# Performance work log

Measured on AMD Instinct MI355X. Metric: run time of the kernel, lower is better.

## Reference

```python
import jax, jax.numpy as jnp
from jax import lax
import numpy as np

B, C_IN, H, W = 8, 1024, 64, 64
DI, C_OUT = 512, 1024
BN_EPS = 1e-5


def setup_inputs() -> dict:
    key = jax.random.key(0)
    ks = jax.random.split(key, 5)
    std = 0.01  # torch init.normal_(std=0.01)
    return {
        "x": jax.random.normal(ks[0], (B, C_IN, H, W), jnp.float32),
        "theta_w": jax.random.normal(ks[1], (DI, C_IN), jnp.float32) * std,
        "theta_b": jnp.zeros((DI,), jnp.float32),
        "phi_w": jax.random.normal(ks[2], (DI, C_IN), jnp.float32) * std,
        "phi_b": jnp.zeros((DI,), jnp.float32),
        "g_w": jax.random.normal(ks[3], (DI, C_IN), jnp.float32) * std,
        "g_b": jnp.zeros((DI,), jnp.float32),
        "out_w": jax.random.normal(ks[4], (C_OUT, DI), jnp.float32) * std,
        "out_b": jnp.zeros((C_OUT,), jnp.float32),
        "bn_w": jnp.ones((C_OUT,), jnp.float32),
        "bn_b": jnp.zeros((C_OUT,), jnp.float32),
    }


def _conv1x1(x, w, b):
    # x: [b,c,h,w], w: [o,c] -> [b,o,h,w]
    return jnp.einsum('bchw,oc->bohw', x, w) + b[None, :, None, None]


def reference(x, theta_w, theta_b, phi_w, phi_b, g_w, g_b, out_w, out_b, bn_w, bn_b):
    b, c, h, w = x.shape
    di = theta_w.shape[0]

    theta = _conv1x1(x, theta_w, theta_b).reshape(b, di, h * w)  # [b,di,N]

    # MaxPool2d(kernel=2, stride=2)
    pool = lax.reduce_window(x, -jnp.inf, lax.max,
                             (1, 1, 2, 2), (1, 1, 2, 2), 'VALID')
    phi = _conv1x1(pool, phi_w, phi_b).reshape(b, di, -1)   # [b,di,M]
    g = _conv1x1(pool, g_w, g_b).reshape(b, di, -1)          # [b,di,M]

    # scaled dot-product attention: scores [b,N,M]
    scores = jnp.einsum('bdn,bdm->bnm', theta, phi) * (di ** -0.5)
    p = jax.nn.softmax(scores, axis=-1)

    # t_x = g @ p^T  -> [b,di,N]
    t = jnp.einsum('bdm,bnm->bdn', g, p).reshape(b, di, h, w)

    y = _conv1x1(t, out_w, out_b)  # [b,C_out,h,w]

    # BatchNorm2d (training mode: batch statistics, biased variance)
    mean = jnp.mean(y, axis=(0, 2, 3), keepdims=True)
    var = jnp.var(y, axis=(0, 2, 3), keepdims=True)
    y = (y - mean) * lax.rsqrt(var + BN_EPS)
    y = y * bn_w[None, :, None, None] + bn_b[None, :, None, None]

    return y + x
```

## Files before the change

kernel.cpp:

```cpp
#include <hip/hip_runtime.h>
#include <cstdint>

typedef unsigned short u16;
typedef __attribute__((ext_vector_type(4))) unsigned short u16x4;
typedef __attribute__((ext_vector_type(8))) short short8;
typedef __attribute__((ext_vector_type(4))) float f32x4;

#define DI 512
#define CIN 1024
#define NPIX 4096
#define MPIX 1024

__device__ __forceinline__ float bf2f(u16 u) {
  union { unsigned int i; float f; } v; v.i = ((unsigned int)u) << 16; return v.f;
}
__device__ __forceinline__ u16 f2bf(float f) {
  union { float f; unsigned int i; } v; v.f = f;
  unsigned int r = v.i + 0x7fffu + ((v.i >> 16) & 1u);
  return (u16)(r >> 16);
}
__device__ __forceinline__ void unpack8(uint4 v, float* f) {
  union { unsigned int i; float f; } u;
  u.i = v.x << 16;          f[0] = u.f;
  u.i = v.x & 0xffff0000u;  f[1] = u.f;
  u.i = v.y << 16;          f[2] = u.f;
  u.i = v.y & 0xffff0000u;  f[3] = u.f;
  u.i = v.z << 16;          f[4] = u.f;
  u.i = v.z & 0xffff0000u;  f[5] = u.f;
  u.i = v.w << 16;          f[6] = u.f;
  u.i = v.w & 0xffff0000u;  f[7] = u.f;
}

__device__ __forceinline__ void gload16(const u16* g, u16* l) {
  __builtin_amdgcn_global_load_lds(
      (const __attribute__((address_space(1))) void*)g,
      (__attribute__((address_space(3))) void*)l, 16, 0, 0);
}

template<int N> __device__ __forceinline__ void wait_vmcnt() {
  asm volatile("s_waitcnt vmcnt(%0)" :: "n"(N) : "memory");
}
__device__ __forceinline__ void phase_begin() {
  __builtin_amdgcn_s_barrier();
  __builtin_amdgcn_sched_barrier(0);
  asm volatile("" ::: "memory");
}
__device__ __forceinline__ void phase_end() {
  asm volatile("s_waitcnt lgkmcnt(0)" ::: "memory");
  __builtin_amdgcn_sched_barrier(0);
  __builtin_amdgcn_s_barrier();
  __builtin_amdgcn_sched_barrier(0);
}

__global__ __launch_bounds__(256) void cvt4_kernel(
    const float* __restrict__ s0, const float* __restrict__ s1,
    const float* __restrict__ s2, const float* __restrict__ s3,
    u16* __restrict__ d0, u16* __restrict__ d1,
    u16* __restrict__ d2, u16* __restrict__ d3) {
  int i = blockIdx.x * 256 + threadIdx.x;
  int sel = i >> 17;
  int j = i & 131071;
  const float* src = sel == 0 ? s0 : sel == 1 ? s1 : sel == 2 ? s2 : s3;
  u16* dst = sel == 0 ? d0 : sel == 1 ? d1 : sel == 2 ? d2 : d3;
  float4 v = *(const float4*)(src + (long)j * 4);
  u16x4 w;
  w[0] = f2bf(v.x); w[1] = f2bf(v.y); w[2] = f2bf(v.z); w[3] = f2bf(v.w);
  *(u16x4*)(dst + (long)j * 4) = w;
}

__global__ __launch_bounds__(256) void transpose_pool_kernel(
    const float* __restrict__ x, u16* __restrict__ xT, u16* __restrict__ poolT) {
  __shared__ u16 tile[64][136];
  const int b = blockIdx.z;
  const int n0 = blockIdx.x * 128, c0 = blockIdx.y * 64;
  const float* xb = x + (long)b * CIN * NPIX;
  u16* xTb = xT + (long)b * NPIX * CIN;
  const int t = threadIdx.x;
  const int tc = t >> 5, tn = (t & 31) * 4;
  #pragma unroll
  for (int i = 0; i < 8; i++) {
    int c = tc + i * 8;
    float4 v = *(const float4*)(xb + (long)(c0 + c) * NPIX + n0 + tn);
    u16x4 w;
    w[0] = f2bf(v.x); w[1] = f2bf(v.y); w[2] = f2bf(v.z); w[3] = f2bf(v.w);
    *(u16x4*)&tile[c][tn] = w;
  }
  __syncthreads();
  const int tn2 = t >> 4, tc2 = (t & 15) * 4;
  #pragma unroll
  for (int i = 0; i < 8; i++) {
    int n = tn2 + i * 16;
    u16x4 w;
    w[0] = tile[tc2 + 0][n];
    w[1] = tile[tc2 + 1][n];
    w[2] = tile[tc2 + 2][n];
    w[3] = tile[tc2 + 3][n];
    *(u16x4*)(xTb + (long)(n0 + n) * CIN + c0 + tc2) = w;
  }
  const int j = t & 31, g = t >> 5;
  u16 r[8] __attribute__((aligned(16)));
  #pragma unroll
  for (int k = 0; k < 8; k++) {
    const int c = g * 8 + k;
    const unsigned d0 = *(const unsigned*)&tile[c][2 * j];
    const unsigned d1 = *(const unsigned*)&tile[c][64 + 2 * j];
    float m0 = fmaxf(bf2f((u16)(d0 & 0xffffu)), bf2f((u16)(d0 >> 16)));
    float m1 = fmaxf(bf2f((u16)(d1 & 0xffffu)), bf2f((u16)(d1 >> 16)));
    r[k] = f2bf(fmaxf(m0, m1));
  }
  *(uint4*)(poolT + ((long)b * MPIX + blockIdx.x * 32 + j) * CIN + c0 + g * 8) =
      *(uint4*)r;
}

template<int OM, bool HAS_BIAS, bool HAS_SHIFT, bool HAS_EXP, bool HAS_PSUM2,
         bool HAS_CSP>
__global__ __launch_bounds__(512, 2)
void gemm256(const u16* __restrict__ A, const u16* __restrict__ B,
             void* __restrict__ Cv,
             const float* __restrict__ bias, long sBias,
             const float* __restrict__ cs, long sCS,
             const float* __restrict__ shift, long sShift,
             float* __restrict__ psum_out,
             float scale, int M, int N, int K, long sA, long sB, long sC)
{
  A += blockIdx.z * sA;
  B += blockIdx.z * sB;
  if (HAS_BIAS) bias += blockIdx.z * sBias;
  if (HAS_CSP) cs += blockIdx.z * sCS;
  if (HAS_SHIFT) shift += blockIdx.z * sShift;
  const int bm = blockIdx.y * 256, bn = blockIdx.x * 256;
  __shared__ __align__(16) u16 smem[65536];
  __shared__ float psum[4][256];
  __shared__ float psumq[4][256];
  __shared__ float invs[256];
  const int tid = threadIdx.x;
  const int lane = tid & 63, wave = tid >> 6;
  const int wr = wave >> 2, wc = wave & 3;
  const int lr = lane & 15, q = lane >> 4;
  f32x4 acc[8][4] = {};

  if (HAS_CSP) {
    if (tid < 256) {
      float ssum = 0.f;
      #pragma unroll
      for (int xx = 0; xx < 4; xx++) ssum += cs[xx * 4096 + bn + tid];
      invs[tid] = 1.0f / ssum;
    }
    wait_vmcnt<0>();
    __builtin_amdgcn_sched_barrier(0);
  }

  const int srow = 32 * wave + (lane >> 2);
  const int sk = (((lane & 3) ^ ((lane >> 3) & 3))) * 8;
  const u16* Abase = A + ((long)bm + srow) * K + sk;
  const u16* Bbase = B + ((long)bn + srow) * K + sk;
  const int rswz = (q ^ ((lr >> 1) & 3)) * 8;
  const int aoff = (wr * 128 + lr) * 32 + rswz;
  const int boff = 16384 + (wc * 64 + lr) * 32 + rswz;

#define SA(T_, KK_) { const u16* g_ = Abase + (long)(T_) * 64 + (KK_) * 32; \
    u16* d_ = &smem[(((T_) & 1)) * 32768 + (KK_) * 8192 + wave * 1024]; \
    gload16(g_, d_); gload16(g_ + 16 * (long)K, d_ + 512); }
#define SB(T_, KK_) { const u16* g_ = Bbase + (long)(T_) * 64 + (KK_) * 32; \
    u16* d_ = &smem[(((T_) & 1)) * 32768 + 16384 + (KK_) * 8192 + wave * 1024]; \
    gload16(g_, d_); gload16(g_ + 16 * (long)K, d_ + 512); }
#define CQ(SLOT, KK, RI0, LOADBV) { \
    const int qb_ = (SLOT) * 32768 + (KK) * 8192; \
    if (LOADBV) { \
      _Pragma("unroll") \
      for (int ci_ = 0; ci_ < 4; ci_++) \
        bv[ci_] = *(const short8*)&smem[qb_ + boff + ci_ * 512]; \
    } \
    short8 av_[4]; \
    _Pragma("unroll") \
    for (int r_ = 0; r_ < 4; r_++) \
      av_[r_] = *(const short8*)&smem[qb_ + aoff + ((RI0) + r_) * 512]; \
    __builtin_amdgcn_s_setprio(1); \
    _Pragma("unroll") \
    for (int r_ = 0; r_ < 4; r_++) \
      _Pragma("unroll") \
      for (int ci_ = 0; ci_ < 4; ci_++) \
        acc[(RI0) + r_][ci_] = __builtin_amdgcn_mfma_f32_16x16x32_bf16( \
            av_[r_], bv[ci_], acc[(RI0) + r_][ci_], 0, 0, 0); \
    __builtin_amdgcn_s_setprio(0); }
#define PH(VM, STG, SLOT, KK, RI0, LOADBV) \
    STG; wait_vmcnt<VM>(); phase_begin(); CQ(SLOT, KK, RI0, LOADBV); phase_end();

  const int niter2 = K >> 7;
  short8 bv[4];

  SA(0, 0); SB(0, 0); SA(0, 1); SB(0, 1); SA(1, 0); SB(1, 0);

  for (int u = 0; u < niter2 - 1; ++u) {
    const int t1 = 2 * u + 1, t2 = 2 * u + 2, t3 = 2 * u + 3;
    PH(10, SA(t1, 1), 0, 0, 0, 1)
    PH(10, SB(t1, 1), 0, 0, 4, 0)
    PH(10, SA(t2, 0), 0, 1, 0, 1)
    PH(10, SB(t2, 0), 0, 1, 4, 0)
    PH(10, SA(t2, 1), 1, 0, 0, 1)
    PH(10, SB(t2, 1), 1, 0, 4, 0)
    PH(10, SA(t3, 0), 1, 1, 0, 1)
    PH(10, SB(t3, 0), 1, 1, 4, 0)
  }
  {
    const int t1 = 2 * (niter2 - 1) + 1;
    PH(10, SA(t1, 1), 0, 0, 0, 1)
    PH(10, SB(t1, 1), 0, 0, 4, 0)
    PH(8,  ((void)0), 0, 1, 0, 1)
    PH(6,  ((void)0), 0, 1, 4, 0)
    PH(4,  ((void)0), 1, 0, 0, 1)
    PH(2,  ((void)0), 1, 0, 4, 0)
    PH(0,  ((void)0), 1, 1, 0, 1)
    PH(0,  ((void)0), 1, 1, 4, 0)
  }
#undef SA
#undef SB
#undef CQ
#undef PH

  __syncthreads();

  const int dr = (lane >> 4) * 4;
  float invc[4];
  if (HAS_CSP) {
    #pragma unroll
    for (int ci = 0; ci < 4; ci++) invc[ci] = invs[wc * 64 + ci * 16 + lr];
  }
  float rowsum[8][4], rowsq[8][4];
  if (HAS_EXP || HAS_PSUM2) {
    #pragma unroll
    for (int ri = 0; ri < 8; ri++)
      #pragma unroll
      for (int r = 0; r < 4; r++) { rowsum[ri][r] = 0.f; rowsq[ri][r] = 0.f; }
  }
  #pragma unroll
  for (int ri = 0; ri < 8; ri++) {
    const int rowl = wr * 128 + ri * 16 + dr;
    const int rowb = bm + rowl;
    float bvs[4] = {0.f, 0.f, 0.f, 0.f};
    float shv[4] = {0.f, 0.f, 0.f, 0.f};
    if (HAS_BIAS) {
      #pragma unroll
      for (int r = 0; r < 4; r++) bvs[r] = bias[rowb + r];
    }
    if (HAS_SHIFT) {
      #pragma unroll
      for (int r = 0; r < 4; r++) shv[r] = shift[rowb + r];
    }
    #pragma unroll
    for (int ci = 0; ci < 4; ci++) {
      const int coll = wc * 64 + ci * 16 + lr;
      float v[4];
      #pragma unroll
      for (int r = 0; r < 4; r++) {
        float tv = acc[ri][ci][r] * scale;
        if (HAS_CSP) tv *= invc[ci];
        if (HAS_SHIFT) tv -= shv[r];
        if (HAS_BIAS) tv += bvs[r];
        if (HAS_EXP) tv = expf(tv);
        if (HAS_EXP || HAS_PSUM2) rowsum[ri][r] += tv;
        if (HAS_PSUM2) rowsq[ri][r] += tv * tv;
        v[r] = tv;
      }
      if (OM == 1) {
        u16x4 w;
        #pragma unroll
        for (int r = 0; r < 4; r++) w[r] = f2bf(v[r]);
        unsigned bo = (unsigned)((coll * 256 + rowl) * 2) ^ ((coll & 7) << 4);
        *(u16x4*)((char*)smem + bo) = w;
      } else {
        #pragma unroll
        for (int r = 0; r < 4; r++) smem[(rowl + r) * 256 + coll] = f2bf(v[r]);
      }
    }
  }
  if (HAS_EXP || HAS_PSUM2) {
    #pragma unroll
    for (int msk = 1; msk < 16; msk <<= 1)
      #pragma unroll
      for (int ri = 0; ri < 8; ri++)
        #pragma unroll
        for (int r = 0; r < 4; r++) {
          rowsum[ri][r] += __shfl_xor(rowsum[ri][r], msk);
          if (HAS_PSUM2) rowsq[ri][r] += __shfl_xor(rowsq[ri][r], msk);
        }
    if ((lane & 15) == 0) {
      #pragma unroll
      for (int ri = 0; ri < 8; ri++)
        #pragma unroll
        for (int r = 0; r < 4; r++) {
          psum[wc][wr * 128 + ri * 16 + dr + r] = rowsum[ri][r];
          if (HAS_PSUM2) psumq[wc][wr * 128 + ri * 16 + dr + r] = rowsq[ri][r];
        }
    }
  }
  __syncthreads();
  u16* C = (u16*)Cv + blockIdx.z * sC;
  if (OM == 1) {
    #pragma unroll
    for (int i = 0; i < 16; i++) {
      const int chunk = i * 512 + tid;
      const int coll = chunk >> 5, rq = chunk & 31;
      unsigned bo = (unsigned)(coll * 512 + rq * 16) ^ ((coll & 7) << 4);
      uint4 w = *(const uint4*)((const char*)smem + bo);
      *(uint4*)(C + (long)(bn + coll) * M + bm + rq * 8) = w;
    }
  } else {
    #pragma unroll
    for (int i = 0; i < 16; i++) {
      const int chunk = i * 512 + tid;
      const int row = chunk >> 5, cq = chunk & 31;
      uint4 w = *(const uint4*)(smem + row * 256 + cq * 8);
      *(uint4*)(C + (long)(bm + row) * N + bn + cq * 8) = w;
    }
  }
  if ((HAS_EXP || HAS_PSUM2) && tid < 256) {
    if (HAS_EXP)
      psum_out[((long)blockIdx.z * gridDim.x + blockIdx.x) * 4096 + bm + tid] =
          psum[0][tid] + psum[1][tid] + psum[2][tid] + psum[3][tid];
    if (HAS_PSUM2) {
      const long blk = ((long)blockIdx.z * gridDim.y + blockIdx.y) * gridDim.x
                       + blockIdx.x;
      psum_out[blk * 512 + tid] =
          psum[0][tid] + psum[1][tid] + psum[2][tid] + psum[3][tid];
      psum_out[blk * 512 + 256 + tid] =
          psumq[0][tid] + psumq[1][tid] + psumq[2][tid] + psumq[3][tid];
    }
  }
}

template<int OM, bool HAS_BIAS, bool HAS_CS, bool HAS_SHIFT, bool HAS_EXP,
         bool HAS_PSUM2, bool HAS_CSP>
__global__ __launch_bounds__(256)
void gemm_tn(const u16* __restrict__ A, const u16* __restrict__ B,
             void* __restrict__ Cv, void* __restrict__ Cv2,
             const float* __restrict__ bias, const float* __restrict__ bias2,
             long sBias,
             const float* __restrict__ cs, long sCS,
             const float* __restrict__ shift, long sShift,
             float* __restrict__ psum_out,
             float scale, int M, int N, int K, long sA, long sB, long sC)
{
  A += blockIdx.z * sA;
  B += blockIdx.z * sB;
  if (HAS_BIAS) bias += blockIdx.z * sBias;
  if (HAS_CS || HAS_CSP) cs += blockIdx.z * sCS;
  if (HAS_SHIFT) shift += blockIdx.z * sShift;
  const int bm = blockIdx.y * 128;
  const int bn = blockIdx.x * 128;
  __shared__ __align__(16) u16 smem[128 * 128];
  u16* As = smem;
  u16* Bs = smem + 128 * 64;
  __shared__ float psum[4][128];
  const int tid = threadIdx.x;
  const int lane = tid & 63;
  const int wave = tid >> 6;
  const int wm = (wave >> 1) * 64;
  const int wn = (wave & 1) * 64;
  const int lr = lane & 15;
  const int q  = lane >> 4;
  const int sxor = lane & 7;
  const bool gps = (OM == 3) && (bm >= 512);
  f32x4 acc[4][4] = {};

  if (HAS_CSP) {
    if (tid < 128) {
      float s = 0.f;
      #pragma unroll
      for (int xx = 0; xx < 8; xx++) s += cs[xx * 4096 + bn + tid];
      psum[0][tid] = 1.0f / s;
    }
  }

  const int swz = ((lane & 7) ^ (lane >> 3)) * 8;
  const long grow = 32 * wave + (lane >> 3);
  const u16* Ag = A + ((long)bm + grow) * K + swz;
  const u16* Bg = B + ((long)bn + grow) * K + swz;

  for (int kt = 0; kt < K; kt += 64) {
    __syncthreads();
    #pragma unroll
    for (int i = 0; i < 4; i++) {
      gload16(Ag + (long)(8 * i) * K + kt, &As[(wave * 4 + i) * 512]);
      gload16(Bg + (long)(8 * i) * K + kt, &Bs[(wave * 4 + i) * 512]);
    }
    __syncthreads();
    #pragma unroll
    for (int kk = 0; kk < 2; kk++) {
      short8 av[4], bv[4];
      #pragma unroll
      for (int mi = 0; mi < 4; mi++)
        av[mi] = *(const short8*)&As[(wm + mi * 16 + lr) * 64 +
                                     (((kk << 2) + q) ^ sxor) * 8];
      #pragma unroll
      for (int ni = 0; ni < 4; ni++)
        bv[ni] = *(const short8*)&Bs[(wn + ni * 16 + lr) * 64 +
                                     (((kk << 2) + q) ^ sxor) * 8];
      #pragma unroll
      for (int mi = 0; mi < 4; mi++) {
        #pragma unroll
        for (int ni = 0; ni < 4; ni++)
          acc[mi][ni] = __builtin_amdgcn_mfma_f32_16x16x32_bf16(
              av[mi], bv[ni], acc[mi][ni], 0, 0, 0);
      }
    }
  }

  float invc[4];
  if (HAS_CSP) {
    #pragma unroll
    for (int ni = 0; ni < 4; ni++) invc[ni] = psum[0][wn + ni * 16 + lr];
  }
  __syncthreads();
  const int dr = (lane >> 4) * 4;
  const bool trans_out = (OM == 1) || (OM == 3 && !gps);
  float rowsum[4][4];
  float rowsq[4][4];
  if (HAS_EXP || HAS_PSUM2 || gps) {
    #pragma unroll
    for (int mi = 0; mi < 4; mi++)
      #pragma unroll
      for (int r = 0; r < 4; r++) { rowsum[mi][r] = 0.f; rowsq[mi][r] = 0.f; }
  }
  const float* bp = (OM == 3 && gps) ? bias2 - 512 : bias;
  #pragma unroll
  for (int mi = 0; mi < 4; mi++) {
    const int rowl = wm + mi * 16 + dr;
    const int rowb = bm + rowl;
    float bvs[4] = {0.f, 0.f, 0.f, 0.f};
    float shv[4] = {0.f, 0.f, 0.f, 0.f};
    if (HAS_BIAS) {
      #pragma unroll
      for (int r = 0; r < 4; r++) bvs[r] = bp[rowb + r];
    }
    if (HAS_SHIFT) {
      #pragma unroll
      for (int r = 0; r < 4; r++) shv[r] = shift[rowb + r];
    }
    #pragma unroll
    for (int ni = 0; ni < 4; ni++) {
      const int coll = wn + ni * 16 + lr;
      const float csv = HAS_CSP ? invc[ni] : (HAS_CS ? cs[bn + coll] : 1.0f);
      float v[4];
      #pragma unroll
      for (int r = 0; r < 4; r++) {
        float t = acc[mi][ni][r] * scale;
        if (HAS_CS || HAS_CSP) t *= csv;
        if (HAS_SHIFT) t -= shv[r];
        if (HAS_BIAS) t += bvs[r];
        if (HAS_EXP) t = expf(t);
        if (HAS_EXP || HAS_PSUM2 || gps) rowsum[mi][r] += t;
        if (HAS_PSUM2) rowsq[mi][r] += t * t;
        v[r] = t;
      }
      if (trans_out) {
        u16x4 w;
        #pragma unroll
        for (int r = 0; r < 4; r++) w[r] = f2bf(v[r]);
        unsigned bo = (unsigned)((coll * 128 + rowl) * 2) ^ ((coll & 7) << 4);
        *(u16x4*)((char*)smem + bo) = w;
      } else {
        #pragma unroll
        for (int r = 0; r < 4; r++) smem[(rowl + r) * 128 + coll] = f2bf(v[r]);
      }
    }
  }
  if (HAS_EXP || HAS_PSUM2 || gps) {
    #pragma unroll
    for (int msk = 1; msk < 16; msk <<= 1)
      #pragma unroll
      for (int mi = 0; mi < 4; mi++)
        #pragma unroll
        for (int r = 0; r < 4; r++) {
          rowsum[mi][r] += __shfl_xor(rowsum[mi][r], msk);
          if (HAS_PSUM2) rowsq[mi][r] += __shfl_xor(rowsq[mi][r], msk);
        }
    if ((lane & 15) == 0) {
      #pragma unroll
      for (int mi = 0; mi < 4; mi++)
        #pragma unroll
        for (int r = 0; r < 4; r++) {
          psum[wave & 1][wm + mi * 16 + dr + r] = rowsum[mi][r];
          if (HAS_PSUM2) psum[2 + (wave & 1)][wm + mi * 16 + dr + r] = rowsq[mi][r];
        }
    }
  }
  __syncthreads();
  if (trans_out) {
    const int Ms = (OM == 3) ? 512 : M;
    u16* C = (u16*)Cv + blockIdx.z * sC;
    #pragma unroll
    for (int i = 0; i < 8; i++) {
      const int chunk = i * 256 + tid;
      const int coll = chunk >> 4, rq = chunk & 15;
      unsigned bo = (unsigned)(coll * 256 + rq * 16) ^ ((coll & 7) << 4);
      uint4 w = *(const uint4*)((const char*)smem + bo);
      *(uint4*)(C + (long)(bn + coll) * Ms + bm + rq * 8) = w;
    }
  } else {
    u16* C = (OM == 3) ? (u16*)Cv2 + blockIdx.z * sC : (u16*)Cv + blockIdx.z * sC;
    const int rbase = (OM == 3) ? bm - 512 : bm;
    #pragma unroll
    for (int i = 0; i < 8; i++) {
      const int chunk = i * 256 + tid;
      const int row = chunk >> 4, cq = chunk & 15;
      uint4 w = *(const uint4*)(smem + row * 128 + cq * 8);
      *(uint4*)(C + (long)(rbase + row) * N + bn + cq * 8) = w;
    }
  }
  if (HAS_EXP || HAS_PSUM2 || gps) {
    if (tid < 128) {
      if (HAS_EXP)
        psum_out[((long)blockIdx.z * gridDim.x + blockIdx.x) * 4096 + bm + tid] =
            psum[0][tid] + psum[1][tid];
      if (HAS_PSUM2) {
        const long blk = ((long)blockIdx.z * gridDim.y + blockIdx.y) * gridDim.x
                         + blockIdx.x;
        psum_out[blk * 256 + tid] = psum[0][tid] + psum[1][tid];
        psum_out[blk * 256 + 128 + tid] = psum[2][tid] + psum[3][tid];
      }
      if (gps)
        psum_out[((long)blockIdx.z * gridDim.x + blockIdx.x) * 512 +
                 (bm - 512) + tid] = psum[0][tid] + psum[1][tid];
    }
  }
}

__global__ __launch_bounds__(256) void gbar_kernel(const float* __restrict__ g_ps,
                                                   float* __restrict__ gbar) {
  const int idx = blockIdx.x * 256 + threadIdx.x;
  const int b = idx >> 9, d = idx & 511;
  const float* p = g_ps + (long)b * 8 * 512 + d;
  float s = 0.f;
  #pragma unroll
  for (int xx = 0; xx < 8; xx++) s += p[(long)xx * 512];
  gbar[idx] = s * (1.0f / 1024.0f);
}

__global__ __launch_bounds__(256) void c0_kernel(const float* __restrict__ out_w,
                                                 const float* __restrict__ out_b,
                                                 const float* __restrict__ gbar,
                                                 float* __restrict__ c0) {
  const int idx = blockIdx.x * 4 + (threadIdx.x >> 6);
  const int lane = threadIdx.x & 63;
  const int b = idx >> 10, c = idx & 1023;
  const int d0 = lane * 8;
  float4 w0 = *(const float4*)(out_w + (long)c * DI + d0);
  float4 w1 = *(const float4*)(out_w + (long)c * DI + d0 + 4);
  float4 g0 = *(const float4*)(gbar + (long)b * DI + d0);
  float4 g1 = *(const float4*)(gbar + (long)b * DI + d0 + 4);
  float s = w0.x * g0.x + w0.y * g0.y + w0.z * g0.z + w0.w * g0.w
          + w1.x * g1.x + w1.y * g1.y + w1.z * g1.z + w1.w * g1.w;
  #pragma unroll
  for (int off = 32; off > 0; off >>= 1) s += __shfl_xor(s, off);
  if (lane == 0) c0[idx] = out_b[c] + s;
}

__global__ __launch_bounds__(256) void stats2_kernel(const float* __restrict__ partial,
                                                     const float* __restrict__ c0,
                                                     float* __restrict__ stats) {
  const int co = blockIdx.x * 256 + threadIdx.x;
  const int by = co >> 8, r = co & 255;
  float sd = 0.f, sd2 = 0.f, sbc = 0.f;
  for (int b = 0; b < 8; b++) {
    float sb = 0.f, qb = 0.f;
    #pragma unroll
    for (int bx = 0; bx < 16; bx++) {
      const long blk = (((long)b * 4 + by) * 16 + bx) * 512;
      sb += partial[blk + r];
      qb += partial[blk + 256 + r];
    }
    sd += sb; sd2 += qb;
    sbc += c0[b * 1024 + co] * sb;
  }
  float sc0 = 0.f, sc02 = 0.f;
  #pragma unroll
  for (int b = 0; b < 8; b++) {
    float c = c0[b * 1024 + co];
    sc0 += c; sc02 += c * c;
  }
  stats[co] = 4096.0f * sc0 + sd;
  stats[1024 + co] = 4096.0f * sc02 + 2.0f * sbc + sd2;
}

__global__ __launch_bounds__(256) void final_kernel(const u16* __restrict__ dy,
    const float* __restrict__ x, const float* __restrict__ stats,
    const float* __restrict__ c0,
    const float* __restrict__ bnw, const float* __restrict__ bnb,
    float* __restrict__ out) {
  const int bc = blockIdx.x;
  const int co = bc & 1023;
  const float mean = stats[co] * (1.0f / 32768.0f);
  const float var = stats[1024 + co] * (1.0f / 32768.0f) - mean * mean;
  const float inv = rsqrtf(var + 1e-5f) * bnw[co];
  const float addc = bnb[co] - mean * inv + c0[bc] * inv;
  const long base = (long)bc * 4096;
  const int t = threadIdx.x;
  #pragma unroll
  for (int i = 0; i < 2; i++) {
    const long off = base + (long)(i * 256 + t) * 8;
    uint4 v = *(const uint4*)(dy + off);
    float f[8]; unpack8(v, f);
    const float4 x0 = *(const float4*)(x + off);
    const float4 x1 = *(const float4*)(x + off + 4);
    float4 o0, o1;
    o0.x = f[0] * inv + addc + x0.x;
    o0.y = f[1] * inv + addc + x0.y;
    o0.z = f[2] * inv + addc + x0.z;
    o0.w = f[3] * inv + addc + x0.w;
    o1.x = f[4] * inv + addc + x1.x;
    o1.y = f[5] * inv + addc + x1.y;
    o1.z = f[6] * inv + addc + x1.z;
    o1.w = f[7] * inv + addc + x1.w;
    *(float4*)(out + off) = o0;
    *(float4*)(out + off + 4) = o1;
  }
}

extern "C" void kernel_launch(void* const* d_in, const int* in_sizes, int n_in,
                              void* d_out, int out_size, void* d_ws, size_t ws_size,
                              hipStream_t stream) {
  (void)in_sizes; (void)n_in; (void)out_size; (void)ws_size;
  const float* x       = (const float*)d_in[0];
  const float* theta_w = (const float*)d_in[1];
  const float* theta_b = (const float*)d_in[2];
  const float* phi_w   = (const float*)d_in[3];
  const float* phi_b   = (const float*)d_in[4];
  const float* g_w     = (const float*)d_in[5];
  const float* g_b     = (const float*)d_in[6];
  const float* out_w   = (const float*)d_in[7];
  const float* out_b   = (const float*)d_in[8];
  const float* bn_w    = (const float*)d_in[9];
  const float* bn_b    = (const float*)d_in[10];
  float* out = (float*)d_out;
  char* ws = (char*)d_ws;
  const size_t MB = 1024 * 1024;

  u16* xT     = (u16*)(ws + 0 * MB);
  u16* poolT  = (u16*)(ws + 64 * MB);
  u16* w_th   = (u16*)(ws + 80 * MB);
  u16* w_ph   = (u16*)(ws + 81 * MB);
  u16* w_g    = (u16*)(ws + 82 * MB);
  u16* thetaT = (u16*)(ws + 84 * MB);
  u16* phiT   = (u16*)(ws + 116 * MB);
  u16* g_n    = (u16*)(ws + 124 * MB);
  u16* e      = (u16*)(ws + 132 * MB);
  u16* tT     = (u16*)(ws + 196 * MB);
  u16* w_out  = (u16*)(ws + 228 * MB);
  float* gbar  = (float*)(ws + 229 * MB);
  float* c0b   = (float*)(ws + 229 * MB + 16384);
  float* stats = (float*)(ws + 229 * MB + 49152);
  float* partial = (float*)(ws + 230 * MB);
  float* partial2 = (float*)(ws + 231 * MB);
  float* g_ps = (float*)(ws + 233 * MB);
  u16* dy = xT;

  cvt4_kernel<<<2048, 256, 0, stream>>>(theta_w, phi_w, g_w, out_w,
                                        w_th, w_ph, w_g, w_out);
  transpose_pool_kernel<<<dim3(32, 16, 8), 256, 0, stream>>>(x, xT, poolT);
  gemm256<1, true, false, false, false, false>
      <<<dim3(16, 2, 8), 512, 0, stream>>>(
      w_th, xT, thetaT, theta_b, 0L, nullptr, 0L, nullptr, 0L, nullptr,
      1.0f, 512, 4096, 1024, 0L, (long)NPIX * CIN, (long)NPIX * DI);
  gemm_tn<3, true, false, false, false, false, false>
      <<<dim3(8, 8, 8), 256, 0, stream>>>(
      w_ph, poolT, phiT, g_n, phi_b, g_b, 0L, nullptr, 0L, nullptr, 0L,
      g_ps, 1.0f, 1024, 1024, 1024, 0L, (long)MPIX * CIN, (long)MPIX * DI);
  gbar_kernel<<<16, 256, 0, stream>>>(g_ps, gbar);
  c0_kernel<<<2048, 256, 0, stream>>>(out_w, out_b, gbar, c0b);
  gemm256<0, false, false, true, false, false>
      <<<dim3(4, 16, 8), 512, 0, stream>>>(
      thetaT, phiT, e, nullptr, 0L, nullptr, 0L, nullptr, 0L, partial,
      0.044194173824159216f, 4096, 1024, 512,
      (long)NPIX * DI, (long)MPIX * DI, (long)NPIX * MPIX);
  gemm256<1, false, true, false, false, true>
      <<<dim3(16, 2, 8), 512, 0, stream>>>(
      g_n, e, tT, nullptr, 0L, partial, 16384L, gbar, 512L, nullptr,
      1.0f, 512, 4096, 1024,
      (long)DI * MPIX, (long)NPIX * MPIX, (long)NPIX * DI);
  gemm256<0, false, false, false, true, false>
      <<<dim3(16, 4, 8), 512, 0, stream>>>(
      w_out, tT, dy, nullptr, 0L, nullptr, 0L, nullptr, 0L, partial2,
      1.0f, 1024, 4096, 512, 0L, (long)NPIX * DI, (long)1024 * NPIX);
  stats2_kernel<<<4, 256, 0, stream>>>(partial2, c0b, stats);
  final_kernel<<<8192, 256, 0, stream>>>(dy, x, stats, c0b, bn_w, bn_b, out);
}
```

Baseline: 344.7 us.

## Fuse BN stats reduction into final kernel, swizzle epilogue LDS, use fast exp

Removes the separate stats2 launch. Each final_kernel block now reduces its channel's partial sums and sums of squares with wave shuffles, then broadcasts the scale and shift through shared memory. The row-major epilogue staging in both GEMM kernels gets an XOR swizzle on the column index to reduce LDS bank conflicts, and expf is replaced with __expf in the softmax-exp epilogue. The trade is redundant stats work: each of the 8192 blocks repeats its channel's reduction, so every channel is reduced 8 times, and it adds two block barriers before the elementwise pass.

Result: faster. 337.8 us (-2.0%).

```diff
diff --git a/kernel.cpp b/kernel.cpp
--- a/kernel.cpp
+++ b/kernel.cpp
@@ -257,7 +257,7 @@
         if (HAS_CSP) tv *= invc[ci];
         if (HAS_SHIFT) tv -= shv[r];
         if (HAS_BIAS) tv += bvs[r];
-        if (HAS_EXP) tv = expf(tv);
+        if (HAS_EXP) tv = __expf(tv);
         if (HAS_EXP || HAS_PSUM2) rowsum[ri][r] += tv;
         if (HAS_PSUM2) rowsq[ri][r] += tv * tv;
         v[r] = tv;
@@ -270,7 +270,10 @@
         *(u16x4*)((char*)smem + bo) = w;
       } else {
         #pragma unroll
-        for (int r = 0; r < 4; r++) smem[(rowl + r) * 256 + coll] = f2bf(v[r]);
+        for (int r = 0; r < 4; r++) {
+          const int row = rowl + r;
+          smem[row * 256 + (coll ^ (((row >> 2) & 3) << 4))] = f2bf(v[r]);
+        }
       }
     }
   }
@@ -310,7 +313,8 @@
     for (int i = 0; i < 16; i++) {
       const int chunk = i * 512 + tid;
       const int row = chunk >> 5, cq = chunk & 31;
-      uint4 w = *(const uint4*)(smem + row * 256 + cq * 8);
+      const int cbase = (cq * 8) ^ (((row >> 2) & 3) << 4);
+      uint4 w = *(const uint4*)(smem + row * 256 + cbase);
       *(uint4*)(C + (long)(bm + row) * N + bn + cq * 8) = w;
     }
   }
@@ -448,7 +452,7 @@
         if (HAS_CS || HAS_CSP) t *= csv;
         if (HAS_SHIFT) t -= shv[r];
         if (HAS_BIAS) t += bvs[r];
-        if (HAS_EXP) t = expf(t);
+        if (HAS_EXP) t = __expf(t);
         if (HAS_EXP || HAS_PSUM2 || gps) rowsum[mi][r] += t;
         if (HAS_PSUM2) rowsq[mi][r] += t * t;
         v[r] = t;
@@ -461,7 +465,10 @@
         *(u16x4*)((char*)smem + bo) = w;
       } else {
         #pragma unroll
-        for (int r = 0; r < 4; r++) smem[(rowl + r) * 128 + coll] = f2bf(v[r]);
+        for (int r = 0; r < 4; r++) {
+          const int row = rowl + r;
+          smem[row * 128 + (coll ^ (((row >> 2) & 3) << 4))] = f2bf(v[r]);
+        }
       }
     }
   }
@@ -504,7 +511,8 @@
     for (int i = 0; i < 8; i++) {
       const int chunk = i * 256 + tid;
       const int row = chunk >> 4, cq = chunk & 15;
-      uint4 w = *(const uint4*)(smem + row * 128 + cq * 8);
+      const int cbase = (cq * 8) ^ (((row >> 2) & 3) << 4);
+      uint4 w = *(const uint4*)(smem + row * 128 + cbase);
       *(uint4*)(C + (long)(rbase + row) * N + bn + cq * 8) = w;
     }
   }
@@ -556,46 +564,57 @@
   if (lane == 0) c0[idx] = out_b[c] + s;
 }
 
-__global__ __launch_bounds__(256) void stats2_kernel(const float* __restrict__ partial,
-                                                     const float* __restrict__ c0,
-                                                     float* __restrict__ stats) {
-  const int co = blockIdx.x * 256 + threadIdx.x;
-  const int by = co >> 8, r = co & 255;
-  float sd = 0.f, sd2 = 0.f, sbc = 0.f;
-  for (int b = 0; b < 8; b++) {
-    float sb = 0.f, qb = 0.f;
-    #pragma unroll
-    for (int bx = 0; bx < 16; bx++) {
-      const long blk = (((long)b * 4 + by) * 16 + bx) * 512;
-      sb += partial[blk + r];
-      qb += partial[blk + 256 + r];
-    }
-    sd += sb; sd2 += qb;
-    sbc += c0[b * 1024 + co] * sb;
-  }
-  float sc0 = 0.f, sc02 = 0.f;
-  #pragma unroll
-  for (int b = 0; b < 8; b++) {
-    float c = c0[b * 1024 + co];
-    sc0 += c; sc02 += c * c;
-  }
-  stats[co] = 4096.0f * sc0 + sd;
-  stats[1024 + co] = 4096.0f * sc02 + 2.0f * sbc + sd2;
-}
-
 __global__ __launch_bounds__(256) void final_kernel(const u16* __restrict__ dy,
-    const float* __restrict__ x, const float* __restrict__ stats,
+    const float* __restrict__ x, const float* __restrict__ partial,
     const float* __restrict__ c0,
     const float* __restrict__ bnw, const float* __restrict__ bnb,
     float* __restrict__ out) {
+  __shared__ float red[6];
+  __shared__ float bcast[2];
   const int bc = blockIdx.x;
   const int co = bc & 1023;
-  const float mean = stats[co] * (1.0f / 32768.0f);
-  const float var = stats[1024 + co] * (1.0f / 32768.0f) - mean * mean;
-  const float inv = rsqrtf(var + 1e-5f) * bnw[co];
-  const float addc = bnb[co] - mean * inv + c0[bc] * inv;
+  const int t = threadIdx.x;
+  if (t < 128) {
+    const int b2 = t >> 4, bx = t & 15;
+    const int by = co >> 8, r = co & 255;
+    const long blk = (((long)b2 * 4 + by) * 16 + bx) * 512;
+    float s = partial[blk + r];
+    float qq = partial[blk + 256 + r];
+    #pragma unroll
+    for (int off = 1; off < 16; off <<= 1) {
+      s += __shfl_xor(s, off);
+      qq += __shfl_xor(qq, off);
+    }
+    float sbc = c0[b2 * 1024 + co] * s;
+    #pragma unroll
+    for (int off = 16; off < 64; off <<= 1) {
+      s += __shfl_xor(s, off);
+      qq += __shfl_xor(qq, off);
+      sbc += __shfl_xor(sbc, off);
+    }
+    if (t == 0)  { red[0] = s; red[1] = qq; red[2] = sbc; }
+    if (t == 64) { red[3] = s; red[4] = qq; red[5] = sbc; }
+  }
+  __syncthreads();
+  if (t == 0) {
+    float sdT = red[0] + red[3], sd2T = red[1] + red[4], sbcT = red[2] + red[5];
+    float sc0 = 0.f, sc02 = 0.f;
+    #pragma unroll
+    for (int bb = 0; bb < 8; bb++) {
+      float c = c0[bb * 1024 + co];
+      sc0 += c; sc02 += c * c;
+    }
+    float S = 4096.0f * sc0 + sdT;
+    float S2 = 4096.0f * sc02 + 2.0f * sbcT + sd2T;
+    float mean = S * (1.0f / 32768.0f);
+    float var = S2 * (1.0f / 32768.0f) - mean * mean;
+    float inv = rsqrtf(var + 1e-5f) * bnw[co];
+    bcast[0] = inv;
+    bcast[1] = bnb[co] - mean * inv + c0[bc] * inv;
+  }
+  __syncthreads();
+  const float inv = bcast[0], addc = bcast[1];
   const long base = (long)bc * 4096;
-  const int t = threadIdx.x;
   #pragma unroll
   for (int i = 0; i < 2; i++) {
     const long off = base + (long)(i * 256 + t) * 8;
@@ -649,7 +668,6 @@
   u16* w_out  = (u16*)(ws + 228 * MB);
   float* gbar  = (float*)(ws + 229 * MB);
   float* c0b   = (float*)(ws + 229 * MB + 16384);
-  float* stats = (float*)(ws + 229 * MB + 49152);
   float* partial = (float*)(ws + 230 * MB);
   float* partial2 = (float*)(ws + 231 * MB);
   float* g_ps = (float*)(ws + 233 * MB);
@@ -682,6 +700,5 @@
       <<<dim3(16, 4, 8), 512, 0, stream>>>(
       w_out, tT, dy, nullptr, 0L, nullptr, 0L, nullptr, 0L, partial2,
       1.0f, 1024, 4096, 512, 0L, (long)NPIX * DI, (long)1024 * NPIX);
-  stats2_kernel<<<4, 256, 0, stream>>>(partial2, c0b, stats);
-  final_kernel<<<8192, 256, 0, stream>>>(dy, x, stats, c0b, bn_w, bn_b, out);
-}
+  final_kernel<<<8192, 256, 0, stream>>>(dy, x, partial2, c0b, bn_w, bn_b, out);
+}
```
